# Kernel tuning notes

Hardware: AMD Instinct MI355X
Metric: run time of the kernel (lower is better)

The kernel has to match this reference:

```python
import jax, jax.numpy as jnp
import numpy as np

DIM = 1024
NUM_HEADS = 16
HEAD_DIM = DIM // NUM_HEADS
SCALE = HEAD_DIM ** -0.5


def setup_inputs() -> dict:
    key0 = jax.random.key(0)
    ks = jax.random.split(key0, 8)
    B, L, S = 2, 1024, 2048
    inp = {
        "query": jax.random.normal(ks[0], (B, L, DIM), dtype=jnp.float32),
        "key": jax.random.normal(ks[1], (B, S, DIM), dtype=jnp.float32),
        "value": jax.random.normal(ks[2], (B, S, DIM), dtype=jnp.float32),
        # projection weights, stored as [in, out] so x @ W matches torch Linear
        "Wq": jax.random.normal(ks[3], (DIM, DIM), dtype=jnp.float32) * (DIM ** -0.5),
        "Wk": jax.random.normal(ks[4], (DIM, DIM), dtype=jnp.float32) * (DIM ** -0.5),
        "Wv": jax.random.normal(ks[5], (DIM, DIM), dtype=jnp.float32) * (DIM ** -0.5),
        "Wo": jax.random.normal(ks[6], (DIM, DIM), dtype=jnp.float32) * (DIM ** -0.5),
        "bo": jax.random.normal(ks[7], (DIM,), dtype=jnp.float32) * 0.02,
    }
    return inp


def reference(query, key, value, Wq, Wk, Wv, Wo, bo):
    B, L, C = query.shape
    S = key.shape[1]
    H, D = NUM_HEADS, HEAD_DIM
    # QKV projections (no bias), split heads: [B, H, L/S, D]
    q = (query @ Wq).reshape(B, L, H, D).transpose(0, 2, 1, 3)
    k = (key @ Wk).reshape(B, S, H, D).transpose(0, 2, 1, 3)
    v = (value @ Wv).reshape(B, S, H, D).transpose(0, 2, 1, 3)
    # scaled dot-product attention (qk_norm=False -> identity)
    attn = jnp.einsum("bhld,bhsd->bhls", q * SCALE, k)
    attn = jax.nn.softmax(attn, axis=-1)
    x = jnp.einsum("bhls,bhsd->bhld", attn, v)
    x = x.transpose(0, 2, 1, 3).reshape(B, L, C)
    # output projection (with bias)
    return x @ Wo + bo
```

## Files before the change

kernel.cpp:

```cpp
#include <hip/hip_runtime.h>

namespace {

typedef _Float16 f16;
typedef __attribute__((ext_vector_type(2))) _Float16 f16x2;
typedef __attribute__((ext_vector_type(4))) _Float16 f16x4;
typedef __attribute__((ext_vector_type(8))) _Float16 f16x8;
typedef __attribute__((ext_vector_type(4))) float f32x4;
typedef __attribute__((ext_vector_type(16))) float f32x16;

constexpr int kDim   = 1024;
constexpr int kHeads = 16;
constexpr int kHd    = 64;
constexpr int kB     = 2;
constexpr int kL     = 1024;
constexpr int kS     = 2048;

struct PrepArgs {
  const float* csrc[3];
  f16* cdst[3];
  int cn[3];
  const float* w[4];
  f16* wt[4];
};

__global__ __launch_bounds__(256) void prep(PrepArgs a) {
  __shared__ float T[32][33];
  const int y = blockIdx.y;
  if (y < 3) {
    const int i = (blockIdx.x * 256 + threadIdx.x) * 8;
    if (i >= a.cn[y]) return;
    const float* __restrict__ src = a.csrc[y];
    float4 v0 = *(const float4*)(src + i);
    float4 v1 = *(const float4*)(src + i + 4);
    f16x8 h = {(f16)v0.x, (f16)v0.y, (f16)v0.z, (f16)v0.w,
               (f16)v1.x, (f16)v1.y, (f16)v1.z, (f16)v1.w};
    *(f16x8*)(a.cdst[y] + i) = h;
  } else {
    if (blockIdx.x >= 1024) return;
    const int z = y - 3;
    const float* __restrict__ W = a.w[z];
    f16* __restrict__ Wt = a.wt[z];
    const int n0 = (blockIdx.x & 31) * 32;
    const int k0 = (blockIdx.x >> 5) * 32;
    const int r = threadIdx.x >> 3;
    const int c = (threadIdx.x & 7) * 4;
    float4 v = *(const float4*)(W + (size_t)(k0 + r) * kDim + n0 + c);
    T[c + 0][r] = v.x; T[c + 1][r] = v.y; T[c + 2][r] = v.z; T[c + 3][r] = v.w;
    __syncthreads();
    f16x4 h = {(f16)T[r][c], (f16)T[r][c + 1], (f16)T[r][c + 2], (f16)T[r][c + 3]};
    *(f16x4*)(Wt + (size_t)(n0 + r) * kDim + k0 + c) = h;
  }
}

struct ProjArgs {
  const f16* A[3];
  const f16* Bt[3];
  f16* C[3];
};

__global__ __launch_bounds__(256) void gemm_proj(ProjArgs p) {
  constexpr int K = kDim;
  constexpr int NI = K / 32;
  int bx = blockIdx.x;
  int z, m0, n0, Nz;
  if (bx < 128)      { z = 0; m0 = (bx >> 3) * 128; n0 = (bx & 7) * 128; Nz = kDim; }
  else if (bx < 384) { bx -= 128; z = 1; m0 = (bx >> 3) * 128; n0 = (bx & 7) * 128; Nz = kDim; }
  else               { bx -= 384; z = 2; m0 = (bx >> 5) * 128; n0 = (bx & 31) * 128; Nz = kB * kS; }
  const f16* __restrict__ A  = p.A[z];
  const f16* __restrict__ Bt = p.Bt[z];
  f16* __restrict__ C = p.C[z];

  __shared__ __align__(16) f16 As[2][128 * 32];
  __shared__ __align__(16) f16 Bs[2][128 * 32];
  const int t = threadIdx.x;
  const int lane = t & 63;
  const int wave = t >> 6;
  const int wm = (wave >> 1) * 64;
  const int wn = (wave & 1) * 64;
  const int col = lane & 15;
  const int quad = lane >> 4;

  f32x4 acc[4][4];
#pragma unroll
  for (int i = 0; i < 4; ++i)
#pragma unroll
    for (int j = 0; j < 4; ++j) acc[i][j] = (f32x4){0.f, 0.f, 0.f, 0.f};

  const int c0 = t, c1 = t + 256;
  const f16* a0 = A + (size_t)(m0 + (c0 >> 2)) * K + (c0 & 3) * 8;
  const f16* a1 = A + (size_t)(m0 + (c1 >> 2)) * K + (c1 & 3) * 8;
  const f16* b0 = Bt + (size_t)(n0 + (c0 >> 2)) * K + (c0 & 3) * 8;
  const f16* b1 = Bt + (size_t)(n0 + (c1 >> 2)) * K + (c1 & 3) * 8;

  {
    f16x8 ra0 = *(const f16x8*)(a0);
    f16x8 ra1 = *(const f16x8*)(a1);
    f16x8 rb0 = *(const f16x8*)(b0);
    f16x8 rb1 = *(const f16x8*)(b1);
    *(f16x8*)(As[0] + c0 * 8) = ra0;
    *(f16x8*)(As[0] + c1 * 8) = ra1;
    *(f16x8*)(Bs[0] + c0 * 8) = rb0;
    *(f16x8*)(Bs[0] + c1 * 8) = rb1;
  }

  for (int i = 0; i < NI; ++i) {
    const int cur = i & 1;
    f16x8 na0, na1, nb0, nb1;
    if (i + 1 < NI) {
      const int ko = (i + 1) * 32;
      na0 = *(const f16x8*)(a0 + ko);
      na1 = *(const f16x8*)(a1 + ko);
      nb0 = *(const f16x8*)(b0 + ko);
      nb1 = *(const f16x8*)(b1 + ko);
    }
    __syncthreads();

    f16x8 af[4], bf[4];
#pragma unroll
    for (int mt = 0; mt < 4; ++mt)
      af[mt] = *(const f16x8*)(As[cur] + (wm + mt * 16 + col) * 32 + quad * 8);
#pragma unroll
    for (int nt = 0; nt < 4; ++nt)
      bf[nt] = *(const f16x8*)(Bs[cur] + (wn + nt * 16 + col) * 32 + quad * 8);
#pragma unroll
    for (int mt = 0; mt < 4; ++mt)
#pragma unroll
      for (int nt = 0; nt < 4; ++nt)
        acc[mt][nt] = __builtin_amdgcn_mfma_f32_16x16x32_f16(
            af[mt], bf[nt], acc[mt][nt], 0, 0, 0);

    if (i + 1 < NI) {
      const int nxt = 1 - cur;
      *(f16x8*)(As[nxt] + c0 * 8) = na0;
      *(f16x8*)(As[nxt] + c1 * 8) = na1;
      *(f16x8*)(Bs[nxt] + c0 * 8) = nb0;
      *(f16x8*)(Bs[nxt] + c1 * 8) = nb1;
    }
  }

  const int crow = m0 + wm + quad * 4;
  const int ccol = n0 + wn + col;
#pragma unroll
  for (int mt = 0; mt < 4; ++mt)
#pragma unroll
    for (int nt = 0; nt < 4; ++nt)
#pragma unroll
      for (int r = 0; r < 4; ++r)
        C[(size_t)(crow + mt * 16 + r) * Nz + ccol + nt * 16] =
            (f16)acc[mt][nt][r];
}

__global__ __launch_bounds__(256) void gemm_out(
    const f16* __restrict__ A, const f16* __restrict__ Bt,
    const float* __restrict__ bias, float* __restrict__ C, int M, int N, int K)
{
  __shared__ __align__(16) f16 As[2][64 * 32];
  __shared__ __align__(16) f16 Bs[2][64 * 32];
  const int t = threadIdx.x;
  const int lane = t & 63;
  const int wave = t >> 6;
  const int n0 = blockIdx.x * 64;
  const int m0 = blockIdx.y * 64;
  const int wm = (wave >> 1) * 32;
  const int wn = (wave & 1) * 32;
  const int col = lane & 15;
  const int quad = lane >> 4;
  const int NI = K / 32;

  f32x4 acc[2][2];
#pragma unroll
  for (int i = 0; i < 2; ++i)
#pragma unroll
    for (int j = 0; j < 2; ++j) acc[i][j] = (f32x4){0.f, 0.f, 0.f, 0.f};

  const f16* a0 = A + (size_t)(m0 + (t >> 2)) * K + (t & 3) * 8;
  const f16* b0 = Bt + (size_t)(n0 + (t >> 2)) * K + (t & 3) * 8;

  {
    f16x8 ra0 = *(const f16x8*)(a0);
    f16x8 rb0 = *(const f16x8*)(b0);
    *(f16x8*)(As[0] + t * 8) = ra0;
    *(f16x8*)(Bs[0] + t * 8) = rb0;
  }

  for (int i = 0; i < NI; ++i) {
    const int cur = i & 1;
    f16x8 na0, nb0;
    if (i + 1 < NI) {
      const int ko = (i + 1) * 32;
      na0 = *(const f16x8*)(a0 + ko);
      nb0 = *(const f16x8*)(b0 + ko);
    }
    __syncthreads();

    f16x8 af[2], bf[2];
#pragma unroll
    for (int mt = 0; mt < 2; ++mt)
      af[mt] = *(const f16x8*)(As[cur] + (wm + mt * 16 + col) * 32 + quad * 8);
#pragma unroll
    for (int nt = 0; nt < 2; ++nt)
      bf[nt] = *(const f16x8*)(Bs[cur] + (wn + nt * 16 + col) * 32 + quad * 8);
#pragma unroll
    for (int mt = 0; mt < 2; ++mt)
#pragma unroll
      for (int nt = 0; nt < 2; ++nt)
        acc[mt][nt] = __builtin_amdgcn_mfma_f32_16x16x32_f16(
            af[mt], bf[nt], acc[mt][nt], 0, 0, 0);

    if (i + 1 < NI) {
      const int nxt = 1 - cur;
      *(f16x8*)(As[nxt] + t * 8) = na0;
      *(f16x8*)(Bs[nxt] + t * 8) = nb0;
    }
  }

  const int crow = m0 + wm + quad * 4;
  const int ccol = n0 + wn + col;
#pragma unroll
  for (int mt = 0; mt < 2; ++mt)
#pragma unroll
    for (int nt = 0; nt < 2; ++nt) {
      const float bv = bias[ccol + nt * 16];
#pragma unroll
      for (int r = 0; r < 4; ++r)
        C[(size_t)(crow + mt * 16 + r) * N + ccol + nt * 16] =
            acc[mt][nt][r] + bv;
    }
}


__device__ inline unsigned pk2f(float a, float b) {
  union { f16x2 h; unsigned u; } c;
  c.h = f16x2{(f16)a, (f16)b};
  return c.u;
}

__device__ inline void swap32(unsigned& x, unsigned& y) {
  asm("v_permlane32_swap_b32 %0, %1" : "+v"(x), "+v"(y));
}

__global__ __launch_bounds__(256, 2) void flash_attn_mfma4(
    const f16* __restrict__ q, const f16* __restrict__ k,
    const f16* __restrict__ vT, f16* __restrict__ x)
{
  constexpr int LP  = 72;
  constexpr int NT2 = (kS / 2) / 64;
  __shared__ __align__(16) f16 Kt[2][2][64 * LP];
  __shared__ __align__(16) f16 Vt[2][2][64 * LP];

  const int t    = threadIdx.x;
  const int lane = t & 63;
  const int wave = t >> 6;
  const int wq   = wave & 1;
  const int wh   = wave >> 1;
  const int ln   = lane & 31;
  const int hi   = lane >> 5;
  const int bh   = blockIdx.x;
  const int l0   = blockIdx.y * 64;
  const int h    = bh & (kHeads - 1);
  const int b    = bh >> 4;

  f16x8 qf[4];
  {
    const f16* src = q + ((size_t)b * kL + l0 + wq * 32 + ln) * kDim + h * kHd + hi * 8;
#pragma unroll
    for (int ks = 0; ks < 4; ++ks) {
      qf[ks] = *(const f16x8*)(src + ks * 16);
#pragma unroll
      for (int u = 0; u < 8; ++u) qf[ks][u] *= (f16)0.125f;
    }
  }

  const int srow = t >> 2;
  const int scol = (t & 3) * 16;
  const f16* kb = k + ((size_t)b * kS + srow) * kDim + h * kHd + scol;
  const f16* vb = vT + ((size_t)(h * kHd + srow)) * (kB * kS) + b * kS + scol;
  const size_t kHalf = (size_t)1024 * kDim;

  f32x16 accO[2];
#pragma unroll
  for (int dt = 0; dt < 2; ++dt)
#pragma unroll
    for (int r = 0; r < 16; ++r) accO[dt][r] = 0.f;
  float lsum = 0.f;

  f16x8 kh0a, kh0b, kh1a, kh1b, vh0a, vh0b, vh1a, vh1b;

#define STAGE_LOAD(i)                                                   \
  { const f16* kp0 = kb + (size_t)(i) * 64 * kDim;                      \
    const f16* kp1 = kp0 + kHalf;                                       \
    const f16* vp0 = vb + (i) * 64;                                     \
    const f16* vp1 = vp0 + 1024;                                        \
    kh0a = *(const f16x8*)(kp0); kh0b = *(const f16x8*)(kp0 + 8);       \
    kh1a = *(const f16x8*)(kp1); kh1b = *(const f16x8*)(kp1 + 8);       \
    vh0a = *(const f16x8*)(vp0); vh0b = *(const f16x8*)(vp0 + 8);       \
    vh1a = *(const f16x8*)(vp1); vh1b = *(const f16x8*)(vp1 + 8); }

#define STAGE_WRITE(bf)                                                 \
  { f16* kd0 = &Kt[bf][0][srow * LP + scol];                            \
    f16* kd1 = &Kt[bf][1][srow * LP + scol];                            \
    f16* vd0 = &Vt[bf][0][srow * LP + scol];                            \
    f16* vd1 = &Vt[bf][1][srow * LP + scol];                            \
    *(f16x8*)(kd0) = kh0a; *(f16x8*)(kd0 + 8) = kh0b;                   \
    *(f16x8*)(kd1) = kh1a; *(f16x8*)(kd1 + 8) = kh1b;                   \
    *(f16x8*)(vd0) = vh0a; *(f16x8*)(vd0 + 8) = vh0b;                   \
    *(f16x8*)(vd1) = vh1a; *(f16x8*)(vd1 + 8) = vh1b; }

  STAGE_LOAD(0);
  STAGE_WRITE(0);

  for (int i = 0; i < NT2; ++i) {
    const int cur = i & 1;
    if (i + 1 < NT2) STAGE_LOAD(i + 1);
    __syncthreads();

    const f16* Kc = &Kt[cur][wh][0];
    const f16* Vc = &Vt[cur][wh][0];

    f16x8 pf[4];
#pragma unroll
    for (int sub = 0; sub < 2; ++sub) {
      f32x16 s;
#pragma unroll
      for (int r = 0; r < 16; ++r) s[r] = 0.f;
      __builtin_amdgcn_s_setprio(1);
#pragma unroll
      for (int ks = 0; ks < 4; ++ks) {
        f16x8 kf = *(const f16x8*)(Kc + (sub * 32 + ln) * LP + ks * 16 + hi * 8);
        s = __builtin_amdgcn_mfma_f32_32x32x16_f16(kf, qf[ks], s, 0, 0, 0);
      }
      __builtin_amdgcn_s_setprio(0);

      float pp[16];
#pragma unroll
      for (int r = 0; r < 16; ++r) { pp[r] = __expf(s[r]); lsum += pp[r]; }

#pragma unroll
      for (int kk = 0; kk < 2; ++kk) {
        unsigned a0 = pk2f(pp[8 * kk + 0], pp[8 * kk + 1]);
        unsigned a1 = pk2f(pp[8 * kk + 2], pp[8 * kk + 3]);
        unsigned b0 = pk2f(pp[8 * kk + 4], pp[8 * kk + 5]);
        unsigned b1 = pk2f(pp[8 * kk + 6], pp[8 * kk + 7]);
        swap32(a0, b0);
        swap32(a1, b1);
        union { unsigned u[4]; f16x8 v; } w;
        w.u[0] = a0; w.u[1] = a1; w.u[2] = b0; w.u[3] = b1;
        pf[sub * 2 + kk] = w.v;
      }
    }

    __builtin_amdgcn_s_setprio(1);
#pragma unroll
    for (int dt = 0; dt < 2; ++dt)
#pragma unroll
      for (int ks = 0; ks < 4; ++ks) {
        f16x8 vf = *(const f16x8*)(Vc + (dt * 32 + ln) * LP + ks * 16 + hi * 8);
        accO[dt] = __builtin_amdgcn_mfma_f32_32x32x16_f16(pf[ks], vf, accO[dt], 0, 0, 0);
      }
    __builtin_amdgcn_s_setprio(0);

    if (i + 1 < NT2) STAGE_WRITE(1 - cur);
  }
#undef STAGE_LOAD
#undef STAGE_WRITE

  lsum += __shfl_xor(lsum, 32);
  __syncthreads();
  float* sc = (float*)&Kt[0][0][0];
  float* sl = sc + 128 * 33;
  if (wh == 1) {
    float* dst = sc + (wq * 64 + lane) * 33;
#pragma unroll
    for (int dt = 0; dt < 2; ++dt)
#pragma unroll
      for (int r = 0; r < 16; ++r) dst[dt * 16 + r] = accO[dt][r];
    sl[wq * 64 + lane] = lsum;
  }
  __syncthreads();
  if (wh == 0) {
    const float* src = sc + (wq * 64 + lane) * 33;
#pragma unroll
    for (int dt = 0; dt < 2; ++dt)
#pragma unroll
      for (int r = 0; r < 16; ++r) accO[dt][r] += src[dt * 16 + r];
    const float inv = 1.f / (lsum + sl[wq * 64 + lane]);
    const size_t row0 = (size_t)b * kL + l0 + wq * 32;
    f16* xb = x + row0 * kDim + h * kHd + ln;
#pragma unroll
    for (int r = 0; r < 16; ++r) {
      const int qr = (r & 3) + 8 * (r >> 2) + 4 * hi;
      const float invr = __shfl(inv, qr);
      xb[(size_t)qr * kDim]      = (f16)(accO[0][r] * invr);
      xb[(size_t)qr * kDim + 32] = (f16)(accO[1][r] * invr);
    }
  }
}

}

extern "C" void kernel_launch(void* const* d_in, const int* in_sizes, int n_in,
                              void* d_out, int out_size, void* d_ws, size_t ws_size,
                              hipStream_t stream) {
  const float* query = (const float*)d_in[0];
  const float* key   = (const float*)d_in[1];
  const float* value = (const float*)d_in[2];
  const float* Wq    = (const float*)d_in[3];
  const float* Wk    = (const float*)d_in[4];
  const float* Wv    = (const float*)d_in[5];
  const float* Wo    = (const float*)d_in[6];
  const float* bo    = (const float*)d_in[7];
  float* out = (float*)d_out;

  f16* ws = (f16*)d_ws;
  f16* qh  = ws;
  f16* kh  = qh + (size_t)kB * kL * kDim;
  f16* vh  = kh + (size_t)kB * kS * kDim;
  f16* wqt = vh + (size_t)kB * kS * kDim;
  f16* wkt = wqt + (size_t)kDim * kDim;
  f16* wvt = wkt + (size_t)kDim * kDim;
  f16* wot = wvt + (size_t)kDim * kDim;
  f16* qp  = wot + (size_t)kDim * kDim;
  f16* kp  = qp + (size_t)kB * kL * kDim;
  f16* vpT = kp + (size_t)kB * kS * kDim;
  f16* xh  = vpT + (size_t)kB * kS * kDim;

  PrepArgs pr;
  pr.csrc[0] = query; pr.cdst[0] = qh; pr.cn[0] = kB * kL * kDim;
  pr.csrc[1] = key;   pr.cdst[1] = kh; pr.cn[1] = kB * kS * kDim;
  pr.csrc[2] = value; pr.cdst[2] = vh; pr.cn[2] = kB * kS * kDim;
  pr.w[0] = Wq; pr.wt[0] = wqt;
  pr.w[1] = Wk; pr.wt[1] = wkt;
  pr.w[2] = Wv; pr.wt[2] = wvt;
  pr.w[3] = Wo; pr.wt[3] = wot;
  prep<<<dim3(2048, 7), 256, 0, stream>>>(pr);

  ProjArgs pa;
  pa.A[0] = qh;  pa.Bt[0] = wqt; pa.C[0] = qp;
  pa.A[1] = kh;  pa.Bt[1] = wkt; pa.C[1] = kp;
  pa.A[2] = wvt; pa.Bt[2] = vh;  pa.C[2] = vpT;
  gemm_proj<<<dim3(640), 256, 0, stream>>>(pa);

  flash_attn_mfma4<<<dim3(kB * kHeads, kL / 64), 256, 0, stream>>>(
      qp, kp, vpT, xh);

  gemm_out<<<dim3(kDim / 64, (kB * kL) / 64), 256, 0, stream>>>(
      xh, wot, bo, out, kB * kL, kDim, kDim);
}
```

Measured before the change: 178.1 us.

## Use direct global-to-LDS loads and XCD-aware block swizzle in GEMMs

Both projection GEMMs replace the register-staged global-to-shared copies with `global_load_lds` 16-byte direct transfers into the next LDS buffer. Each loop iteration now needs only one barrier, and the VGPRs that held prefetched tiles are freed. Block indices are also remapped so that consecutive blocks on the same XCD work on neighbouring tiles, which is meant to improve L2 reuse. The output GEMM changes to a 1D grid to support the swizzle. The risk is correctness of the LDS DMA ordering: the barrier has to wait on outstanding vector memory loads before the buffer is read.

```diff
diff --git a/kernel.cpp b/kernel.cpp
--- a/kernel.cpp
+++ b/kernel.cpp
@@ -15,6 +15,12 @@
 constexpr int kB     = 2;
 constexpr int kL     = 1024;
 constexpr int kS     = 2048;
+
+__device__ inline void gload16(const f16* g, f16* l) {
+  __builtin_amdgcn_global_load_lds(
+      (const __attribute__((address_space(1))) void*)(g),
+      (__attribute__((address_space(3))) void*)(l), 16, 0, 0);
+}
 
 struct PrepArgs {
   const float* csrc[3];
@@ -62,7 +68,7 @@
 __global__ __launch_bounds__(256) void gemm_proj(ProjArgs p) {
   constexpr int K = kDim;
   constexpr int NI = K / 32;
-  int bx = blockIdx.x;
+  int bx = (blockIdx.x & 7) * 80 + (blockIdx.x >> 3);
   int z, m0, n0, Nz;
   if (bx < 128)      { z = 0; m0 = (bx >> 3) * 128; n0 = (bx & 7) * 128; Nz = kDim; }
   else if (bx < 384) { bx -= 128; z = 1; m0 = (bx >> 3) * 128; n0 = (bx & 7) * 128; Nz = kDim; }
@@ -92,29 +98,28 @@
   const f16* a1 = A + (size_t)(m0 + (c1 >> 2)) * K + (c1 & 3) * 8;
   const f16* b0 = Bt + (size_t)(n0 + (c0 >> 2)) * K + (c0 & 3) * 8;
   const f16* b1 = Bt + (size_t)(n0 + (c1 >> 2)) * K + (c1 & 3) * 8;
-
-  {
-    f16x8 ra0 = *(const f16x8*)(a0);
-    f16x8 ra1 = *(const f16x8*)(a1);
-    f16x8 rb0 = *(const f16x8*)(b0);
-    f16x8 rb1 = *(const f16x8*)(b1);
-    *(f16x8*)(As[0] + c0 * 8) = ra0;
-    *(f16x8*)(As[0] + c1 * 8) = ra1;
-    *(f16x8*)(Bs[0] + c0 * 8) = rb0;
-    *(f16x8*)(Bs[0] + c1 * 8) = rb1;
-  }
+  f16* const as0 = As[0] + c0 * 8;
+  f16* const as1 = As[0] + c1 * 8;
+  f16* const bs0 = Bs[0] + c0 * 8;
+  f16* const bs1 = Bs[0] + c1 * 8;
+  constexpr int kBuf = 128 * 32;
+
+  gload16(a0, as0);
+  gload16(a1, as1);
+  gload16(b0, bs0);
+  gload16(b1, bs1);
+  __syncthreads();
 
   for (int i = 0; i < NI; ++i) {
     const int cur = i & 1;
-    f16x8 na0, na1, nb0, nb1;
     if (i + 1 < NI) {
       const int ko = (i + 1) * 32;
-      na0 = *(const f16x8*)(a0 + ko);
-      na1 = *(const f16x8*)(a1 + ko);
-      nb0 = *(const f16x8*)(b0 + ko);
-      nb1 = *(const f16x8*)(b1 + ko);
-    }
-    __syncthreads();
+      const int nb = (1 - cur) * kBuf;
+      gload16(a0 + ko, as0 + nb);
+      gload16(a1 + ko, as1 + nb);
+      gload16(b0 + ko, bs0 + nb);
+      gload16(b1 + ko, bs1 + nb);
+    }
 
     f16x8 af[4], bf[4];
 #pragma unroll
@@ -130,13 +135,7 @@
         acc[mt][nt] = __builtin_amdgcn_mfma_f32_16x16x32_f16(
             af[mt], bf[nt], acc[mt][nt], 0, 0, 0);
 
-    if (i + 1 < NI) {
-      const int nxt = 1 - cur;
-      *(f16x8*)(As[nxt] + c0 * 8) = na0;
-      *(f16x8*)(As[nxt] + c1 * 8) = na1;
-      *(f16x8*)(Bs[nxt] + c0 * 8) = nb0;
-      *(f16x8*)(Bs[nxt] + c1 * 8) = nb1;
-    }
+    __syncthreads();
   }
 
   const int crow = m0 + wm + quad * 4;
@@ -160,13 +159,15 @@
   const int t = threadIdx.x;
   const int lane = t & 63;
   const int wave = t >> 6;
-  const int n0 = blockIdx.x * 64;
-  const int m0 = blockIdx.y * 64;
+  const int swz = (blockIdx.x & 7) * 64 + (blockIdx.x >> 3);
+  const int n0 = (swz & 15) * 64;
+  const int m0 = (swz >> 4) * 64;
   const int wm = (wave >> 1) * 32;
   const int wn = (wave & 1) * 32;
   const int col = lane & 15;
   const int quad = lane >> 4;
   const int NI = K / 32;
+  constexpr int kBuf = 64 * 32;
 
   f32x4 acc[2][2];
 #pragma unroll
@@ -176,23 +177,21 @@
 
   const f16* a0 = A + (size_t)(m0 + (t >> 2)) * K + (t & 3) * 8;
   const f16* b0 = Bt + (size_t)(n0 + (t >> 2)) * K + (t & 3) * 8;
-
-  {
-    f16x8 ra0 = *(const f16x8*)(a0);
-    f16x8 rb0 = *(const f16x8*)(b0);
-    *(f16x8*)(As[0] + t * 8) = ra0;
-    *(f16x8*)(Bs[0] + t * 8) = rb0;
-  }
+  f16* const as0 = As[0] + t * 8;
+  f16* const bs0 = Bs[0] + t * 8;
+
+  gload16(a0, as0);
+  gload16(b0, bs0);
+  __syncthreads();
 
   for (int i = 0; i < NI; ++i) {
     const int cur = i & 1;
-    f16x8 na0, nb0;
     if (i + 1 < NI) {
       const int ko = (i + 1) * 32;
-      na0 = *(const f16x8*)(a0 + ko);
-      nb0 = *(const f16x8*)(b0 + ko);
-    }
-    __syncthreads();
+      const int nb = (1 - cur) * kBuf;
+      gload16(a0 + ko, as0 + nb);
+      gload16(b0 + ko, bs0 + nb);
+    }
 
     f16x8 af[2], bf[2];
 #pragma unroll
@@ -208,11 +207,7 @@
         acc[mt][nt] = __builtin_amdgcn_mfma_f32_16x16x32_f16(
             af[mt], bf[nt], acc[mt][nt], 0, 0, 0);
 
-    if (i + 1 < NI) {
-      const int nxt = 1 - cur;
-      *(f16x8*)(As[nxt] + t * 8) = na0;
-      *(f16x8*)(Bs[nxt] + t * 8) = nb0;
-    }
+    __syncthreads();
   }
 
   const int crow = m0 + wm + quad * 4;
@@ -444,6 +439,6 @@
   flash_attn_mfma4<<<dim3(kB * kHeads, kL / 64), 256, 0, stream>>>(
       qp, kp, vpT, xh);
 
-  gemm_out<<<dim3(kDim / 64, (kB * kL) / 64), 256, 0, stream>>>(
+  gemm_out<<<dim3(512), 256, 0, stream>>>(
       xh, wot, bo, out, kB * kL, kDim, kDim);
 }
```

Result: no change. 180.6 us (+1.4%).
